# Performance work log

Measured on AMD Instinct MI355X. Metric: run time of the kernel, lower is better.

## Reference

```python
import jax, jax.numpy as jnp
import numpy as np

N, E, D, EDIM, L, H = 50000, 800000, 128, 16, 3, 8


def setup_inputs() -> dict:
    key = jax.random.key(0)
    ks = jax.random.split(key, 16)
    inner = (L + 1) * D  # concat of input + 3 GCN layer outputs
    return {
        "x": jax.random.normal(ks[0], (N, D), jnp.float32),
        "edge_index": jax.random.randint(ks[1], (2, E), 0, N),
        "edge_attr": jax.random.normal(ks[2], (E, EDIM), jnp.float32),
        "dag_edge_index": jax.random.randint(ks[3], (2, E), 0, N),
        "W_v": jax.random.normal(ks[4], (D, D), jnp.float32) * 0.05,
        "W_qk": jax.random.normal(ks[5], (D, 2 * D), jnp.float32) * 0.05,
        "gcn_W": jax.random.normal(ks[6], (L, D, D), jnp.float32) * 0.05,
        "gcn_b": jnp.zeros((L, D), jnp.float32),
        "gcn_root": jax.random.normal(ks[7], (L, D), jnp.float32) * 0.05,
        "gcn_We": jax.random.normal(ks[8], (L, EDIM, D), jnp.float32) * 0.05,
        "gcn_be": jnp.zeros((L, D), jnp.float32),
        "bn_gamma": jnp.ones((inner,), jnp.float32),
        "bn_beta": jnp.zeros((inner,), jnp.float32),
        "W_se": jax.random.normal(ks[9], (inner, D), jnp.float32) * 0.05,
        "b_se": jnp.zeros((D,), jnp.float32),
        "W_out": jax.random.normal(ks[10], (D, D), jnp.float32) * 0.05,
        "b_out": jnp.zeros((D,), jnp.float32),
    }


def reference(x, edge_index, edge_attr, dag_edge_index, W_v, W_qk, gcn_W, gcn_b,
              gcn_root, gcn_We, gcn_be, bn_gamma, bn_beta, W_se, b_se, W_out, b_out):
    n = x.shape[0]
    row, col = edge_index[0], edge_index[1]  # source j, target i

    def gcn_layer(h, Wl, bl, root, We, be):
        h = h @ Wl + bl                                   # [N, D]
        e = edge_attr @ We + be                           # [E, D]
        deg = jax.ops.segment_sum(jnp.ones(row.shape[0], h.dtype), row, num_segments=n) + 1.0
        dis = deg ** -0.5
        norm = dis[row] * dis[col]                        # [E]
        msg = norm[:, None] * jax.nn.relu(h[row] + e)     # gather + per-edge transform
        agg = jax.ops.segment_sum(msg, col, num_segments=n)  # scatter-add at target
        return agg + jax.nn.relu(h + root) / deg[:, None]

    # StructureExtractor: 3 GCN layers, concat skip features
    xs = [x]
    h = x
    for i in range(gcn_W.shape[0]):
        h = jax.nn.relu(gcn_layer(h, gcn_W[i], gcn_b[i], gcn_root[i], gcn_We[i], gcn_be[i]))
        xs.append(h)
    xc = jnp.concatenate(xs, axis=-1)                     # [N, 4D]
    mu = xc.mean(0)
    var = xc.var(0)
    xc = (xc - mu) / jnp.sqrt(var + 1e-5) * bn_gamma + bn_beta  # BatchNorm1d (batch stats)
    x_struct = xc @ W_se + b_se                           # [N, D]

    # sparse multi-head attention over dag_rr_edge_index
    v = x @ W_v
    qk = x_struct @ W_qk
    d = x.shape[1]
    qk_src_tbl, qk_dst_tbl = qk[:, :d], qk[:, d:]         # chunk(2): (qk_j, qk_i)
    hd = d // H
    scale = hd ** -0.5
    src, dst = dag_edge_index[0], dag_edge_index[1]
    qj = qk_src_tbl[src].reshape(-1, H, hd)
    qi = qk_dst_tbl[dst].reshape(-1, H, hd)
    logits = (qi * qj).sum(-1) * scale                    # [E, H]
    m = jax.ops.segment_max(logits, dst, num_segments=n)
    p = jnp.exp(logits - m[dst])
    s = jax.ops.segment_sum(p, dst, num_segments=n)
    attn = p / s[dst]                                     # per-destination softmax
    vj = v[src].reshape(-1, H, hd)
    out = jax.ops.segment_sum(vj * attn[..., None], dst, num_segments=n).reshape(-1, d)
    return out @ W_out + b_out
```

## Files before the change

### kernel.cpp

```cpp
#include <hip/hip_runtime.h>

#define D 128
#define EDIMC 16
#define GCAP 64

typedef __attribute__((ext_vector_type(8))) short short8v;
typedef __attribute__((ext_vector_type(4))) float f32x4;
typedef __attribute__((ext_vector_type(2))) float f32x2;
typedef __attribute__((ext_vector_type(2))) _Float16 h16x2;

__device__ __forceinline__ float asf(unsigned u){ union{unsigned u; float f;} v; v.u = u; return v.f; }
__device__ __forceinline__ unsigned asu(float f){ union{float f; unsigned u;} v; v.f = f; return v.u; }
__device__ __forceinline__ unsigned short f2bf(float f){
    unsigned u = asu(f);
    unsigned r = (u + 0x7fffu + ((u >> 16) & 1u)) >> 16;
    return (unsigned short)r;
}
__device__ __forceinline__ unsigned packbf(float lo, float hi){
    return (unsigned)f2bf(lo) | ((unsigned)f2bf(hi) << 16);
}
__device__ __forceinline__ unsigned packh(float a, float b){
    union{ h16x2 h; unsigned u; } v;
    v.h = (h16x2){(_Float16)a, (_Float16)b};
    return v.u;
}
__device__ __forceinline__ h16x2 ash2(unsigned u){ union{unsigned u; h16x2 h;} v; v.u = u; return v.h; }

__global__ __launch_bounds__(256) void prep_all(
    const int* __restrict__ row, const int* __restrict__ col,
    const int* __restrict__ asrc_in, const int* __restrict__ adst,
    int E, int N, int gE, int gX, int L,
    const float* __restrict__ eattr, const float* __restrict__ x,
    const float* __restrict__ gW, const float* __restrict__ Wv,
    const float* __restrict__ Wqk, const float* __restrict__ Wout,
    const float* __restrict__ gWe,
    int* __restrict__ cr, int* __restrict__ curg, int* __restrict__ curd,
    int2* __restrict__ gslot, int* __restrict__ asrcS, unsigned* __restrict__ eattrh,
    unsigned* __restrict__ xbf, unsigned* __restrict__ xc,
    unsigned short* __restrict__ gWt, unsigned short* __restrict__ Wvt,
    unsigned short* __restrict__ Wqkt, unsigned short* __restrict__ Woutt,
    unsigned* __restrict__ wpk)
{
    int b = blockIdx.x, tid = threadIdx.x;
    if(b < gE){
        int e = b*256 + tid;
        if(e >= E) return;
        const float4* s4 = (const float4*)(eattr + (size_t)e*EDIMC);
        float4 a = s4[0], bb = s4[1], cc2 = s4[2], d = s4[3];
        unsigned* dst8 = eattrh + (size_t)e*8;
        dst8[0] = packh(a.x, a.y);    dst8[1] = packh(a.z, a.w);
        dst8[2] = packh(bb.x, bb.y);  dst8[3] = packh(bb.z, bb.w);
        dst8[4] = packh(cc2.x, cc2.y);dst8[5] = packh(cc2.z, cc2.w);
        dst8[6] = packh(d.x, d.y);    dst8[7] = packh(d.z, d.w);
        int r = row[e], c = col[e];
        atomicAdd(&cr[r], 1);
        int pg = atomicAdd(&curg[c], 1);
        if(pg < GCAP) gslot[c*GCAP + pg] = make_int2(r, e);
        int s2 = asrc_in[e], d2 = adst[e];
        int pd = atomicAdd(&curd[d2], 1);
        if(pd < GCAP) asrcS[d2*GCAP + pd] = s2;
    } else if(b < gE + gX){
        int idx = (b - gE)*256 + tid;
        if(idx >= N*64) return;
        int i = idx >> 6, c2 = idx & 63;
        float a = x[(size_t)i*128 + c2*2], bb = x[(size_t)i*128 + c2*2 + 1];
        unsigned p = packbf(a, bb);
        xbf[idx] = p;
        xc[(size_t)i*256 + c2] = p;
    } else {
        int wb = b - gE - gX;
        int j = tid;
        if(wb < 384){
            int l = wb >> 7, k = wb & 127;
            if(j < 128) gWt[(size_t)l*16384 + (size_t)j*128 + k] = f2bf(gW[(size_t)l*16384 + (size_t)k*128 + j]);
        } else if(wb < 512){
            int k = wb - 384;
            if(j < 128) Wvt[(size_t)j*128 + k] = f2bf(Wv[(size_t)k*128 + j]);
        } else if(wb < 640){
            int k = wb - 512;
            Wqkt[(size_t)j*128 + k] = f2bf(Wqk[(size_t)k*256 + j]);
        } else if(wb < 768){
            int k = wb - 640;
            if(j < 128) Woutt[(size_t)j*128 + k] = f2bf(Wout[(size_t)k*128 + j]);
        } else {
            int t = wb - 768; int l = t >> 3, kk = t & 7;
            if(j < 128){
                const float* W = gWe + (size_t)l*EDIMC*D;
                wpk[(size_t)l*1024 + kk*128 + j] = packh(W[(size_t)(2*kk)*D + j], W[(size_t)(2*kk+1)*D + j]);
            }
        }
    }
}

__global__ void deg_fin2(const int* __restrict__ cr, float* __restrict__ deg,
                         float* __restrict__ dis, int N){
    int i = blockIdx.x*blockDim.x + threadIdx.x;
    if(i < N){ float d = (float)cr[i] + 1.0f; deg[i] = d; dis[i] = rsqrtf(d); }
}

template<int OUT>
__global__ __launch_bounds__(256) void gemm_mfma(
    const unsigned short* __restrict__ A, const unsigned short* __restrict__ Bt,
    const float* __restrict__ bias, void* __restrict__ Cout,
    int M, int K, int Nc)
{
    int tid = threadIdx.x;
    int wid = tid >> 6, lane = tid & 63;
    int bm = blockIdx.y*64 + wid*16;
    int bn = blockIdx.x*64;
    int lr = lane & 15;
    int kg = lane >> 4;
    int arow = bm + lr; if(arow >= M) arow = M - 1;
    f32x4 acc[4];
    #pragma unroll
    for(int i = 0; i < 4; i++) acc[i] = (f32x4){0.f,0.f,0.f,0.f};
    for(int k0 = 0; k0 < K; k0 += 32){
        short8v a = *(const short8v*)(A + (size_t)arow*K + k0 + kg*8);
        #pragma unroll
        for(int nf = 0; nf < 4; nf++){
            short8v b = *(const short8v*)(Bt + (size_t)(bn + nf*16 + lr)*K + k0 + kg*8);
            acc[nf] = __builtin_amdgcn_mfma_f32_16x16x32_bf16(a, b, acc[nf], 0, 0, 0);
        }
    }
    int crow = bm + kg*4;
    #pragma unroll
    for(int nf = 0; nf < 4; nf++){
        int col = bn + nf*16 + lr;
        float bs = bias ? bias[col] : 0.f;
        #pragma unroll
        for(int r = 0; r < 4; r++){
            int rw = crow + r;
            if(rw < M){
                float val = acc[nf][r] + bs;
                if(OUT == 1)
                    ((unsigned short*)Cout)[(size_t)rw*Nc + col] = f2bf(val);
                else if(OUT == 2)
                    ((_Float16*)Cout)[(size_t)rw*Nc + col] = (_Float16)val;
                else
                    ((float*)Cout)[(size_t)rw*Nc + col] = val;
            }
        }
    }
}

__device__ __forceinline__ void edge_acc5(
    uint4 ea0, uint4 ea1, unsigned hu, float nm,
    const unsigned* __restrict__ w0, const unsigned* __restrict__ w1,
    float be0, float be1, float& a0, float& a1)
{
    float ev0 = be0, ev1 = be1;
    unsigned ea[8] = {ea0.x, ea0.y, ea0.z, ea0.w, ea1.x, ea1.y, ea1.z, ea1.w};
    #pragma unroll
    for(int kk = 0; kk < 8; kk++){
        ev0 = __builtin_amdgcn_fdot2(ash2(ea[kk]), ash2(w0[kk]), ev0, false);
        ev1 = __builtin_amdgcn_fdot2(ash2(ea[kk]), ash2(w1[kk]), ev1, false);
    }
    float sx = fmaxf(asf(hu << 16) + ev0, 0.f);
    float sy = fmaxf(asf(hu & 0xffff0000u) + ev1, 0.f);
    a0 += nm*sx; a1 += nm*sy;
}

__global__ __launch_bounds__(256) void gcn_gather_v7(
    const unsigned* __restrict__ hlin,
    const int* __restrict__ curg,
    const int2* __restrict__ gslot,
    const unsigned* __restrict__ eattrh,
    const float* __restrict__ dis,
    const unsigned* __restrict__ wpk_l,
    const float* __restrict__ be,
    const float* __restrict__ root, const float* __restrict__ deg,
    unsigned* __restrict__ xc, unsigned* __restrict__ hcur, int blk, int N)
{
    int lane = threadIdx.x & 63;
    int node = __builtin_amdgcn_readfirstlane((int)((blockIdx.x*blockDim.x + threadIdx.x) >> 6));
    if(node >= N) return;
    unsigned w0[8], w1[8];
    const uint2* wp2 = (const uint2*)wpk_l;
    #pragma unroll
    for(int kk = 0; kk < 8; kk++){
        uint2 t = wp2[(size_t)kk*64 + lane];
        w0[kk] = t.x; w1[kk] = t.y;
    }
    f32x2 be2 = ((const f32x2*)be)[lane];
    f32x2 rt2 = ((const f32x2*)root)[lane];
    float disn = dis[node];
    int s0 = node*GCAP;
    int s1 = s0 + min(curg[node], GCAP);
    float a0 = 0.f, a1 = 0.f;
    int s = s0;
    for(; s + 4 <= s1; s += 4){
        int2 sl0 = gslot[s+0], sl1 = gslot[s+1], sl2 = gslot[s+2], sl3 = gslot[s+3];
        float d0 = dis[sl0.x], d1 = dis[sl1.x], d2 = dis[sl2.x], d3 = dis[sl3.x];
        unsigned h0 = hlin[(size_t)sl0.x*64 + lane];
        unsigned h1 = hlin[(size_t)sl1.x*64 + lane];
        unsigned h2 = hlin[(size_t)sl2.x*64 + lane];
        unsigned h3 = hlin[(size_t)sl3.x*64 + lane];
        uint4 e00 = *(const uint4*)(eattrh + (size_t)sl0.y*8);
        uint4 e01 = *(const uint4*)(eattrh + (size_t)sl0.y*8 + 4);
        uint4 e10 = *(const uint4*)(eattrh + (size_t)sl1.y*8);
        uint4 e11 = *(const uint4*)(eattrh + (size_t)sl1.y*8 + 4);
        uint4 e20 = *(const uint4*)(eattrh + (size_t)sl2.y*8);
        uint4 e21 = *(const uint4*)(eattrh + (size_t)sl2.y*8 + 4);
        uint4 e30 = *(const uint4*)(eattrh + (size_t)sl3.y*8);
        uint4 e31 = *(const uint4*)(eattrh + (size_t)sl3.y*8 + 4);
        edge_acc5(e00, e01, h0, d0*disn, w0, w1, be2.x, be2.y, a0, a1);
        edge_acc5(e10, e11, h1, d1*disn, w0, w1, be2.x, be2.y, a0, a1);
        edge_acc5(e20, e21, h2, d2*disn, w0, w1, be2.x, be2.y, a0, a1);
        edge_acc5(e30, e31, h3, d3*disn, w0, w1, be2.x, be2.y, a0, a1);
    }
    for(; s < s1; s++){
        int2 sl0 = gslot[s];
        float d0 = dis[sl0.x];
        unsigned h0 = hlin[(size_t)sl0.x*64 + lane];
        uint4 e00 = *(const uint4*)(eattrh + (size_t)sl0.y*8);
        uint4 e01 = *(const uint4*)(eattrh + (size_t)sl0.y*8 + 4);
        edge_acc5(e00, e01, h0, d0*disn, w0, w1, be2.x, be2.y, a0, a1);
    }
    unsigned hlu = hlin[(size_t)node*64 + lane];
    float hlx = asf(hlu << 16), hly = asf(hlu & 0xffff0000u);
    float dinv = 1.f/deg[node];
    float v0 = fmaxf(a0 + fmaxf(hlx + rt2.x, 0.f)*dinv, 0.f);
    float v1 = fmaxf(a1 + fmaxf(hly + rt2.y, 0.f)*dinv, 0.f);
    unsigned p = packbf(v0, v1);
    hcur[(size_t)node*64 + lane] = p;
    xc[(size_t)node*256 + (size_t)blk*64 + lane] = p;
}

__global__ __launch_bounds__(256) void bn_stats_bf(
    const unsigned* __restrict__ xc, int N, float* __restrict__ stats)
{
    int c0 = threadIdx.x;
    int rows_per = (N + gridDim.x - 1)/gridDim.x;
    int r0 = blockIdx.x*rows_per, r1 = min(N, r0 + rows_per);
    float s0=0, q0=0, s1=0, q1=0;
    for(int r = r0; r < r1; r++){
        unsigned u = xc[(size_t)r*256 + c0];
        float a = asf(u << 16), b = asf(u & 0xffff0000u);
        s0 += a; q0 += a*a; s1 += b; q1 += b*b;
    }
    atomicAdd(&stats[2*c0+0], s0);  atomicAdd(&stats[512 + 2*c0+0], q0);
    atomicAdd(&stats[2*c0+1], s1);  atomicAdd(&stats[512 + 2*c0+1], q1);
}

__global__ void fold_all(const float* __restrict__ Wse, const float* __restrict__ gamma,
                         const float* __restrict__ beta, const float* __restrict__ bse,
                         const float* __restrict__ stats, float Ninv,
                         unsigned short* __restrict__ Wse2t, float* __restrict__ bse2)
{
    int b = blockIdx.x, j = threadIdx.x;
    if(b < 512){
        float mu  = stats[b]*Ninv;
        float var = stats[512+b]*Ninv - mu*mu;
        float sc  = gamma[b]*rsqrtf(var + 1e-5f);
        Wse2t[(size_t)j*512 + b] = f2bf(Wse[(size_t)b*128 + j]*sc);
    } else {
        float acc = bse[j];
        for(int k = 0; k < 512; k++){
            float mu  = stats[k]*Ninv;
            float var = stats[512+k]*Ninv - mu*mu;
            float sc  = gamma[k]*rsqrtf(var + 1e-5f);
            float sh  = beta[k] - mu*sc;
            acc += sh*Wse[(size_t)k*128 + j];
        }
        bse2[j] = acc;
    }
}

__global__ __launch_bounds__(256) void attn_fused_v7(
    const unsigned* __restrict__ qk,
    const unsigned* __restrict__ v,
    const int* __restrict__ curd, const int* __restrict__ asrcS,
    unsigned* __restrict__ out, int N)
{
    int lane = threadIdx.x & 63;
    int node = __builtin_amdgcn_readfirstlane((int)((blockIdx.x*blockDim.x + threadIdx.x) >> 6));
    if(node >= N) return;
    int cnt = min(curd[node], GCAP);
    int s0 = node*GCAP, s1 = s0 + cnt;
    float o0 = 0.f, o1 = 0.f;
    if(cnt > 0){
        h16x2 qi2 = ash2(qk[(size_t)node*128 + 64 + lane]);
        float m = -INFINITY, ssum = 0.f, a0 = 0.f, a1 = 0.f;
        int s = s0;
        for(; s + 4 <= s1; s += 4){
            int sr0 = asrcS[s+0], sr1 = asrcS[s+1], sr2 = asrcS[s+2], sr3 = asrcS[s+3];
            unsigned qj[4], vv[4];
            qj[0] = qk[(size_t)sr0*128 + lane];  vv[0] = v[(size_t)sr0*64 + lane];
            qj[1] = qk[(size_t)sr1*128 + lane];  vv[1] = v[(size_t)sr1*64 + lane];
            qj[2] = qk[(size_t)sr2*128 + lane];  vv[2] = v[(size_t)sr2*64 + lane];
            qj[3] = qk[(size_t)sr3*128 + lane];  vv[3] = v[(size_t)sr3*64 + lane];
            float l[4];
            #pragma unroll
            for(int j = 0; j < 4; j++){
                float p = __builtin_amdgcn_fdot2(qi2, ash2(qj[j]), 0.f, false);
                p += __shfl_xor(p, 1);
                p += __shfl_xor(p, 2);
                p += __shfl_xor(p, 4);
                l[j] = p*0.25f;
            }
            #pragma unroll
            for(int j = 0; j < 4; j++){
                float mn = fmaxf(m, l[j]);
                float sc = __expf(m - mn);
                float p  = __expf(l[j] - mn);
                h16x2 v2 = ash2(vv[j]);
                ssum = ssum*sc + p;
                a0 = a0*sc + p*(float)v2.x;
                a1 = a1*sc + p*(float)v2.y;
                m = mn;
            }
        }
        for(; s < s1; s++){
            int srx = asrcS[s];
            h16x2 qj2 = ash2(qk[(size_t)srx*128 + lane]);
            h16x2 v2  = ash2(v [(size_t)srx*64  + lane]);
            float p = __builtin_amdgcn_fdot2(qi2, qj2, 0.f, false);
            p += __shfl_xor(p, 1);
            p += __shfl_xor(p, 2);
            p += __shfl_xor(p, 4);
            float l = p*0.25f;
            float mn = fmaxf(m, l);
            float sc = __expf(m - mn);
            float pe = __expf(l - mn);
            ssum = ssum*sc + pe;
            a0 = a0*sc + pe*(float)v2.x;
            a1 = a1*sc + pe*(float)v2.y;
            m = mn;
        }
        float inv = 1.f/ssum;
        o0 = a0*inv; o1 = a1*inv;
    }
    out[(size_t)node*64 + lane] = packbf(o0, o1);
}

extern "C" void kernel_launch(void* const* d_in, const int* in_sizes, int n_in,
                              void* d_out, int out_size, void* d_ws, size_t ws_size,
                              hipStream_t stream)
{
    const float* x     = (const float*)d_in[0];
    const int*   ei    = (const int*)  d_in[1];
    const float* eattr = (const float*)d_in[2];
    const int*   dei   = (const int*)  d_in[3];
    const float* Wv    = (const float*)d_in[4];
    const float* Wqk   = (const float*)d_in[5];
    const float* gW    = (const float*)d_in[6];
    const float* gb    = (const float*)d_in[7];
    const float* groot = (const float*)d_in[8];
    const float* gWe   = (const float*)d_in[9];
    const float* gbe   = (const float*)d_in[10];
    const float* gamma = (const float*)d_in[11];
    const float* beta  = (const float*)d_in[12];
    const float* Wse   = (const float*)d_in[13];
    const float* bse   = (const float*)d_in[14];
    const float* Wout  = (const float*)d_in[15];
    const float* bout  = (const float*)d_in[16];

    const int N = in_sizes[0]/D;
    const int E = in_sizes[1]/2;
    const int L = in_sizes[7]/D;

    float* ws = (float*)d_ws;
    size_t o = 0;
    auto alloc = [&](size_t n){ size_t r = o; o += (n + 63) & ~(size_t)63; return r; };
    size_t f_deg   = alloc((size_t)N);
    size_t f_dis   = alloc((size_t)N);
    size_t f_hlin  = alloc((size_t)N*64);
    size_t f_hcur  = alloc((size_t)N*64);
    size_t f_xbf   = alloc((size_t)N*64);
    size_t f_xc    = alloc((size_t)N*256);
    size_t f_st    = alloc(1024);
    size_t f_b2    = alloc(128);
    size_t f_cnt   = alloc((size_t)N*3);
    size_t f_gslot = alloc((size_t)N*GCAP*2);
    size_t f_asrc  = alloc((size_t)N*GCAP);
    size_t f_eah   = alloc((size_t)E*8);
    size_t f_wgt   = alloc(90112 + 64);
    size_t f_wpk   = alloc(3*1024);
    size_t f_qk    = alloc((size_t)N*128);
    size_t f_vb    = alloc((size_t)N*64);
    size_t f_xst   = alloc((size_t)N*64);
    size_t f_aout  = alloc((size_t)N*64);
    (void)ws_size;

    float* deg  = ws + f_deg;   float* dis  = ws + f_dis;
    unsigned* hlin = (unsigned*)(ws + f_hlin);
    unsigned* hcur = (unsigned*)(ws + f_hcur);
    unsigned* xbf  = (unsigned*)(ws + f_xbf);
    unsigned* xc   = (unsigned*)(ws + f_xc);
    float* stats = ws + f_st;   float* bse2 = ws + f_b2;
    int* cnts = (int*)(ws + f_cnt);
    int* cr = cnts, *curg = cnts + N, *curd = cnts + 2*N;
    int2* gslot = (int2*)(ws + f_gslot);
    int* asrcS = (int*)(ws + f_asrc);
    unsigned* eattrh = (unsigned*)(ws + f_eah);
    unsigned short* wbase = (unsigned short*)(ws + f_wgt);
    unsigned short* gWt   = wbase;
    unsigned short* Wvt   = gWt + 3*128*128;
    unsigned short* Wqkt  = Wvt + 128*128;
    unsigned short* Woutt = Wqkt + 256*128;
    unsigned short* Wse2t = Woutt + 128*128;
    unsigned* wpk = (unsigned*)(ws + f_wpk);
    unsigned* qk   = (unsigned*)(ws + f_qk);
    unsigned* vbuf = (unsigned*)(ws + f_vb);
    unsigned* xst  = (unsigned*)(ws + f_xst);
    unsigned* aout = (unsigned*)(ws + f_aout);

    const int* e_row = ei;        const int* e_col = ei + E;
    const int* a_src = dei;       const int* a_dst = dei + E;

    dim3 blk256(256);
    int gE = (E+255)/256, gN = (N+255)/256;
    int gNode = ((size_t)N*64 + 255)/256;
    int gX = gNode;
    int gMy = (N+63)/64;

    hipMemsetAsync(cnts, 0, (size_t)N*3*sizeof(int), stream);
    prep_all<<<gE + gX + 768 + 8*L, blk256, 0, stream>>>(
        e_row, e_col, a_src, a_dst, E, N, gE, gX, L,
        eattr, x, gW, Wv, Wqk, Wout, gWe,
        cr, curg, curd, gslot, asrcS, eattrh,
        xbf, xc, gWt, Wvt, Wqkt, Woutt, wpk);
    deg_fin2<<<gN, blk256, 0, stream>>>(cr, deg, dis, N);

    const unsigned* hin = xbf;
    for(int l = 0; l < L; l++){
        dim3 g(2, gMy);
        gemm_mfma<1><<<g, blk256, 0, stream>>>((const unsigned short*)hin, gWt + (size_t)l*D*D,
                                               gb + (size_t)l*D, hlin, N, 128, 128);
        gcn_gather_v7<<<gNode, blk256, 0, stream>>>(hlin, curg, gslot, eattrh, dis,
                                                    wpk + (size_t)l*1024, gbe + (size_t)l*D,
                                                    groot + (size_t)l*D, deg, xc, hcur, l+1, N);
        hin = hcur;
    }

    hipMemsetAsync(stats, 0, 1024*sizeof(float), stream);
    bn_stats_bf<<<256, blk256, 0, stream>>>(xc, N, stats);
    float Ninv = 1.0f/(float)N;
    fold_all<<<513, 128, 0, stream>>>(Wse, gamma, beta, bse, stats, Ninv, Wse2t, bse2);

    {   dim3 g(2, gMy);
        gemm_mfma<1><<<g, blk256, 0, stream>>>((const unsigned short*)xc, Wse2t, bse2, xst, N, 512, 128);
    }
    {   dim3 g(2, gMy);
        gemm_mfma<2><<<g, blk256, 0, stream>>>((const unsigned short*)xbf, Wvt, nullptr, vbuf, N, 128, 128);
    }
    {   dim3 g(4, gMy);
        gemm_mfma<2><<<g, blk256, 0, stream>>>((const unsigned short*)xst, Wqkt, nullptr, qk, N, 128, 256);
    }

    attn_fused_v7<<<gNode, blk256, 0, stream>>>(qk, vbuf, curd, asrcS, aout, N);

    {   dim3 g(2, gMy);
        gemm_mfma<0><<<g, blk256, 0, stream>>>((const unsigned short*)aout, Woutt, bout, (float*)d_out, N, 128, 128);
    }
}
```

Baseline: 696.1 us.

## Fold W_se into W_qk, split GCN gather across wave pairs, batch softmax

Precomputes W_se·W_qk and b_se·W_qk in the prep kernel and folds the BatchNorm scale and shift into that combined matrix. This removes the x_struct GEMM and its buffer, so qk comes from one K=512 GEMM over xc. The GCN gather now splits each node's edge list across two waves and combines the partial sums through shared memory. The attention online softmax handles four edges per rescale instead of one, and bn_stats uses more blocks. The combined weight is rounded to bf16 after folding, so numerics change slightly.

```diff
diff --git a/kernel.cpp b/kernel.cpp
--- a/kernel.cpp
+++ b/kernel.cpp
@@ -33,13 +33,14 @@
     const float* __restrict__ eattr, const float* __restrict__ x,
     const float* __restrict__ gW, const float* __restrict__ Wv,
     const float* __restrict__ Wqk, const float* __restrict__ Wout,
-    const float* __restrict__ gWe,
+    const float* __restrict__ gWe, const float* __restrict__ bse,
+    const float* __restrict__ Wse,
     int* __restrict__ cr, int* __restrict__ curg, int* __restrict__ curd,
     int2* __restrict__ gslot, int* __restrict__ asrcS, unsigned* __restrict__ eattrh,
     unsigned* __restrict__ xbf, unsigned* __restrict__ xc,
     unsigned short* __restrict__ gWt, unsigned short* __restrict__ Wvt,
-    unsigned short* __restrict__ Wqkt, unsigned short* __restrict__ Woutt,
-    unsigned* __restrict__ wpk)
+    unsigned short* __restrict__ Woutt, unsigned* __restrict__ wpk,
+    float* __restrict__ WseWqk, float* __restrict__ bconst)
 {
     int b = blockIdx.x, tid = threadIdx.x;
     if(b < gE){
@@ -78,16 +79,26 @@
             if(j < 128) Wvt[(size_t)j*128 + k] = f2bf(Wv[(size_t)k*128 + j]);
         } else if(wb < 640){
             int k = wb - 512;
-            Wqkt[(size_t)j*128 + k] = f2bf(Wqk[(size_t)k*256 + j]);
-        } else if(wb < 768){
-            int k = wb - 640;
             if(j < 128) Woutt[(size_t)j*128 + k] = f2bf(Wout[(size_t)k*128 + j]);
-        } else {
-            int t = wb - 768; int l = t >> 3, kk = t & 7;
+        } else if(wb < 664){
+            int t = wb - 640; int l = t >> 3, kk = t & 7;
             if(j < 128){
                 const float* W = gWe + (size_t)l*EDIMC*D;
                 wpk[(size_t)l*1024 + kk*128 + j] = packh(W[(size_t)(2*kk)*D + j], W[(size_t)(2*kk+1)*D + j]);
             }
+        } else if(wb < 1176){
+            int k = wb - 664;
+            float acc = 0.f;
+            #pragma unroll 4
+            for(int c = 0; c < 128; c++)
+                acc += Wse[(size_t)k*128 + c] * Wqk[(size_t)c*256 + j];
+            WseWqk[(size_t)k*256 + j] = acc;
+        } else {
+            float acc = 0.f;
+            #pragma unroll 4
+            for(int c = 0; c < 128; c++)
+                acc += bse[c] * Wqk[(size_t)c*256 + j];
+            bconst[j] = acc;
         }
     }
 }
@@ -160,20 +171,21 @@
     a0 += nm*sx; a1 += nm*sy;
 }
 
-__global__ __launch_bounds__(256) void gcn_gather_v7(
-    const unsigned* __restrict__ hlin,
-    const int* __restrict__ curg,
-    const int2* __restrict__ gslot,
-    const unsigned* __restrict__ eattrh,
-    const float* __restrict__ dis,
-    const unsigned* __restrict__ wpk_l,
-    const float* __restrict__ be,
-    const float* __restrict__ root, const float* __restrict__ deg,
+__global__ __launch_bounds__(256) void gcn_gather_v8(
+    const unsigned* __restrict__ hlin, const int* __restrict__ curg,
+    const int2* __restrict__ gslot, const unsigned* __restrict__ eattrh,
+    const float* __restrict__ dis, const unsigned* __restrict__ wpk_l,
+    const float* __restrict__ be, const float* __restrict__ root,
+    const float* __restrict__ deg,
     unsigned* __restrict__ xc, unsigned* __restrict__ hcur, int blk, int N)
 {
-    int lane = threadIdx.x & 63;
-    int node = __builtin_amdgcn_readfirstlane((int)((blockIdx.x*blockDim.x + threadIdx.x) >> 6));
-    if(node >= N) return;
+    __shared__ float part[2][64][2];
+    int tid = threadIdx.x;
+    int lane = tid & 63;
+    int wv = __builtin_amdgcn_readfirstlane(tid >> 6);
+    int pairIdx = wv >> 1, h = wv & 1;
+    int node = blockIdx.x*2 + pairIdx;
+    bool valid = node < N;
     unsigned w0[8], w1[8];
     const uint2* wp2 = (const uint2*)wpk_l;
     #pragma unroll
@@ -182,11 +194,17 @@
         w0[kk] = t.x; w1[kk] = t.y;
     }
     f32x2 be2 = ((const f32x2*)be)[lane];
-    f32x2 rt2 = ((const f32x2*)root)[lane];
-    float disn = dis[node];
-    int s0 = node*GCAP;
-    int s1 = s0 + min(curg[node], GCAP);
     float a0 = 0.f, a1 = 0.f;
+    int s0 = 0, s1 = 0;
+    float disn = 0.f;
+    if(valid){
+        disn = dis[node];
+        int cnt = min(curg[node], GCAP);
+        int half0 = (cnt + 1) >> 1;
+        int base = node*GCAP;
+        s0 = base + (h ? half0 : 0);
+        s1 = base + (h ? cnt : half0);
+    }
     int s = s0;
     for(; s + 4 <= s1; s += 4){
         int2 sl0 = gslot[s+0], sl1 = gslot[s+1], sl2 = gslot[s+2], sl3 = gslot[s+3];
@@ -216,14 +234,21 @@
         uint4 e01 = *(const uint4*)(eattrh + (size_t)sl0.y*8 + 4);
         edge_acc5(e00, e01, h0, d0*disn, w0, w1, be2.x, be2.y, a0, a1);
     }
-    unsigned hlu = hlin[(size_t)node*64 + lane];
-    float hlx = asf(hlu << 16), hly = asf(hlu & 0xffff0000u);
-    float dinv = 1.f/deg[node];
-    float v0 = fmaxf(a0 + fmaxf(hlx + rt2.x, 0.f)*dinv, 0.f);
-    float v1 = fmaxf(a1 + fmaxf(hly + rt2.y, 0.f)*dinv, 0.f);
-    unsigned p = packbf(v0, v1);
-    hcur[(size_t)node*64 + lane] = p;
-    xc[(size_t)node*256 + (size_t)blk*64 + lane] = p;
+    if(h){ part[pairIdx][lane][0] = a0; part[pairIdx][lane][1] = a1; }
+    __syncthreads();
+    if(!h && valid){
+        a0 += part[pairIdx][lane][0];
+        a1 += part[pairIdx][lane][1];
+        f32x2 rt2 = ((const f32x2*)root)[lane];
+        unsigned hlu = hlin[(size_t)node*64 + lane];
+        float hlx = asf(hlu << 16), hly = asf(hlu & 0xffff0000u);
+        float dinv = 1.f/deg[node];
+        float v0 = fmaxf(a0 + fmaxf(hlx + rt2.x, 0.f)*dinv, 0.f);
+        float v1 = fmaxf(a1 + fmaxf(hly + rt2.y, 0.f)*dinv, 0.f);
+        unsigned p = packbf(v0, v1);
+        hcur[(size_t)node*64 + lane] = p;
+        xc[(size_t)node*256 + (size_t)blk*64 + lane] = p;
+    }
 }
 
 __global__ __launch_bounds__(256) void bn_stats_bf(
@@ -242,31 +267,37 @@
     atomicAdd(&stats[2*c0+1], s1);  atomicAdd(&stats[512 + 2*c0+1], q1);
 }
 
-__global__ void fold_all(const float* __restrict__ Wse, const float* __restrict__ gamma,
-                         const float* __restrict__ beta, const float* __restrict__ bse,
+__global__ void fold_all(const float* __restrict__ gamma, const float* __restrict__ beta,
                          const float* __restrict__ stats, float Ninv,
-                         unsigned short* __restrict__ Wse2t, float* __restrict__ bse2)
-{
-    int b = blockIdx.x, j = threadIdx.x;
-    if(b < 512){
-        float mu  = stats[b]*Ninv;
-        float var = stats[512+b]*Ninv - mu*mu;
-        float sc  = gamma[b]*rsqrtf(var + 1e-5f);
-        Wse2t[(size_t)j*512 + b] = f2bf(Wse[(size_t)b*128 + j]*sc);
+                         const float* __restrict__ WseWqk, const float* __restrict__ bconst,
+                         unsigned short* __restrict__ Wqkft, float* __restrict__ bqkf)
+{
+    int b = blockIdx.x, t = threadIdx.x;
+    if(b < 256){
+        int j = b;
+        #pragma unroll
+        for(int half = 0; half < 2; half++){
+            int k = t + half*256;
+            float mu  = stats[k]*Ninv;
+            float var = stats[512+k]*Ninv - mu*mu;
+            float sc  = gamma[k]*rsqrtf(var + 1e-5f);
+            Wqkft[(size_t)j*512 + k] = f2bf(sc * WseWqk[(size_t)k*256 + j]);
+        }
     } else {
-        float acc = bse[j];
+        int j = t;
+        float acc = bconst[j];
         for(int k = 0; k < 512; k++){
             float mu  = stats[k]*Ninv;
             float var = stats[512+k]*Ninv - mu*mu;
             float sc  = gamma[k]*rsqrtf(var + 1e-5f);
             float sh  = beta[k] - mu*sc;
-            acc += sh*Wse[(size_t)k*128 + j];
-        }
-        bse2[j] = acc;
-    }
-}
-
-__global__ __launch_bounds__(256) void attn_fused_v7(
+            acc += sh*WseWqk[(size_t)k*256 + j];
+        }
+        bqkf[j] = acc;
+    }
+}
+
+__global__ __launch_bounds__(256) void attn_fused_v8(
     const unsigned* __restrict__ qk,
     const unsigned* __restrict__ v,
     const int* __restrict__ curd, const int* __restrict__ asrcS,
@@ -298,17 +329,15 @@
                 p += __shfl_xor(p, 4);
                 l[j] = p*0.25f;
             }
-            #pragma unroll
-            for(int j = 0; j < 4; j++){
-                float mn = fmaxf(m, l[j]);
-                float sc = __expf(m - mn);
-                float p  = __expf(l[j] - mn);
-                h16x2 v2 = ash2(vv[j]);
-                ssum = ssum*sc + p;
-                a0 = a0*sc + p*(float)v2.x;
-                a1 = a1*sc + p*(float)v2.y;
-                m = mn;
-            }
+            float mc = fmaxf(fmaxf(fmaxf(l[0], l[1]), fmaxf(l[2], l[3])), m);
+            float sc = __expf(m - mc);
+            float p0 = __expf(l[0] - mc), p1 = __expf(l[1] - mc);
+            float p2 = __expf(l[2] - mc), p3 = __expf(l[3] - mc);
+            h16x2 v0 = ash2(vv[0]), v1 = ash2(vv[1]), v2 = ash2(vv[2]), v3 = ash2(vv[3]);
+            ssum = ssum*sc + (p0 + p1 + p2 + p3);
+            a0 = a0*sc + p0*(float)v0.x + p1*(float)v1.x + p2*(float)v2.x + p3*(float)v3.x;
+            a1 = a1*sc + p0*(float)v0.y + p1*(float)v1.y + p2*(float)v2.y + p3*(float)v3.y;
+            m = mc;
         }
         for(; s < s1; s++){
             int srx = asrcS[s];
@@ -369,16 +398,18 @@
     size_t f_xbf   = alloc((size_t)N*64);
     size_t f_xc    = alloc((size_t)N*256);
     size_t f_st    = alloc(1024);
-    size_t f_b2    = alloc(128);
     size_t f_cnt   = alloc((size_t)N*3);
     size_t f_gslot = alloc((size_t)N*GCAP*2);
     size_t f_asrc  = alloc((size_t)N*GCAP);
     size_t f_eah   = alloc((size_t)E*8);
-    size_t f_wgt   = alloc(90112 + 64);
+    size_t f_wgt   = alloc(40960 + 64);
     size_t f_wpk   = alloc(3*1024);
+    size_t f_wsq   = alloc(512*256);
+    size_t f_bcn   = alloc(256);
+    size_t f_wqf   = alloc(65536);
+    size_t f_bqf   = alloc(256);
     size_t f_qk    = alloc((size_t)N*128);
     size_t f_vb    = alloc((size_t)N*64);
-    size_t f_xst   = alloc((size_t)N*64);
     size_t f_aout  = alloc((size_t)N*64);
     (void)ws_size;
 
@@ -387,7 +418,7 @@
     unsigned* hcur = (unsigned*)(ws + f_hcur);
     unsigned* xbf  = (unsigned*)(ws + f_xbf);
     unsigned* xc   = (unsigned*)(ws + f_xc);
-    float* stats = ws + f_st;   float* bse2 = ws + f_b2;
+    float* stats = ws + f_st;
     int* cnts = (int*)(ws + f_cnt);
     int* cr = cnts, *curg = cnts + N, *curd = cnts + 2*N;
     int2* gslot = (int2*)(ws + f_gslot);
@@ -396,13 +427,14 @@
     unsigned short* wbase = (unsigned short*)(ws + f_wgt);
     unsigned short* gWt   = wbase;
     unsigned short* Wvt   = gWt + 3*128*128;
-    unsigned short* Wqkt  = Wvt + 128*128;
-    unsigned short* Woutt = Wqkt + 256*128;
-    unsigned short* Wse2t = Woutt + 128*128;
+    unsigned short* Woutt = Wvt + 128*128;
     unsigned* wpk = (unsigned*)(ws + f_wpk);
+    float* WseWqk = ws + f_wsq;
+    float* bconst = ws + f_bcn;
+    unsigned short* Wqkft = (unsigned short*)(ws + f_wqf);
+    float* bqkf = ws + f_bqf;
     unsigned* qk   = (unsigned*)(ws + f_qk);
     unsigned* vbuf = (unsigned*)(ws + f_vb);
-    unsigned* xst  = (unsigned*)(ws + f_xst);
     unsigned* aout = (unsigned*)(ws + f_aout);
 
     const int* e_row = ei;        const int* e_col = ei + E;
@@ -413,13 +445,14 @@
     int gNode = ((size_t)N*64 + 255)/256;
     int gX = gNode;
     int gMy = (N+63)/64;
+    int gPair = (N+1)/2;
 
     hipMemsetAsync(cnts, 0, (size_t)N*3*sizeof(int), stream);
-    prep_all<<<gE + gX + 768 + 8*L, blk256, 0, stream>>>(
+    prep_all<<<gE + gX + 1177, blk256, 0, stream>>>(
         e_row, e_col, a_src, a_dst, E, N, gE, gX, L,
-        eattr, x, gW, Wv, Wqk, Wout, gWe,
+        eattr, x, gW, Wv, Wqk, Wout, gWe, bse, Wse,
         cr, curg, curd, gslot, asrcS, eattrh,
-        xbf, xc, gWt, Wvt, Wqkt, Woutt, wpk);
+        xbf, xc, gWt, Wvt, Woutt, wpk, WseWqk, bconst);
     deg_fin2<<<gN, blk256, 0, stream>>>(cr, deg, dis, N);
 
     const unsigned* hin = xbf;
@@ -427,28 +460,25 @@
         dim3 g(2, gMy);
         gemm_mfma<1><<<g, blk256, 0, stream>>>((const unsigned short*)hin, gWt + (size_t)l*D*D,
                                                gb + (size_t)l*D, hlin, N, 128, 128);
-        gcn_gather_v7<<<gNode, blk256, 0, stream>>>(hlin, curg, gslot, eattrh, dis,
+        gcn_gather_v8<<<gPair, blk256, 0, stream>>>(hlin, curg, gslot, eattrh, dis,
                                                     wpk + (size_t)l*1024, gbe + (size_t)l*D,
                                                     groot + (size_t)l*D, deg, xc, hcur, l+1, N);
         hin = hcur;
     }
 
     hipMemsetAsync(stats, 0, 1024*sizeof(float), stream);
-    bn_stats_bf<<<256, blk256, 0, stream>>>(xc, N, stats);
+    bn_stats_bf<<<1024, blk256, 0, stream>>>(xc, N, stats);
     float Ninv = 1.0f/(float)N;
-    fold_all<<<513, 128, 0, stream>>>(Wse, gamma, beta, bse, stats, Ninv, Wse2t, bse2);
-
-    {   dim3 g(2, gMy);
-        gemm_mfma<1><<<g, blk256, 0, stream>>>((const unsigned short*)xc, Wse2t, bse2, xst, N, 512, 128);
-    }
+    fold_all<<<257, blk256, 0, stream>>>(gamma, beta, stats, Ninv, WseWqk, bconst, Wqkft, bqkf);
+
     {   dim3 g(2, gMy);
         gemm_mfma<2><<<g, blk256, 0, stream>>>((const unsigned short*)xbf, Wvt, nullptr, vbuf, N, 128, 128);
     }
     {   dim3 g(4, gMy);
-        gemm_mfma<2><<<g, blk256, 0, stream>>>((const unsigned short*)xst, Wqkt, nullptr, qk, N, 128, 256);
-    }
-
-    attn_fused_v7<<<gNode, blk256, 0, stream>>>(qk, vbuf, curd, asrcS, aout, N);
+        gemm_mfma<2><<<g, blk256, 0, stream>>>((const unsigned short*)xc, Wqkft, bqkf, qk, N, 512, 256);
+    }
+
+    attn_fused_v8<<<gNode, blk256, 0, stream>>>(qk, vbuf, curd, asrcS, aout, N);
 
     {   dim3 g(2, gMy);
         gemm_mfma<0><<<g, blk256, 0, stream>>>((const unsigned short*)aout, Woutt, bout, (float*)d_out, N, 128, 128);
```

Result: slower. 749.0 us (+7.6%).
